# Optimization experiments

Hardware: AMD Instinct MI355X
Metric: run time of the kernel (lower is better)

Reference implementation:

```python
import jax, jax.numpy as jnp
import numpy as np

B, S, D, H, E = 4, 1024, 1024, 16, 4
HD = D // H
EPS = 1e-5


def setup_inputs() -> dict:
    key = jax.random.key(0)
    ks = jax.random.split(key, 6)
    std = 0.02
    return {
        "hidden_states": jax.random.normal(ks[0], (B, S, D), dtype=jnp.float32),
        "Wr": jax.random.normal(ks[1], (D, E), dtype=jnp.float32) * std,
        "br": jnp.zeros((E,), jnp.float32),
        "ln_g": jnp.ones((E, D), jnp.float32),
        "ln_b": jnp.zeros((E, D), jnp.float32),
        "W_attn": jax.random.normal(ks[2], (E, D, 3 * D), dtype=jnp.float32) * std,
        "b_attn": jnp.zeros((E, 3 * D), jnp.float32),
        "W_proj": jax.random.normal(ks[3], (E, D, D), dtype=jnp.float32) * std,
        "b_proj": jnp.zeros((E, D), jnp.float32),
    }


def reference(hidden_states, Wr, br, ln_g, ln_b, W_attn, b_attn, W_proj, b_proj):
    b, s, d = hidden_states.shape
    x = hidden_states.reshape(b * s, d)  # [N, D]

    # naive softmax router over experts
    score = jax.nn.softmax(x @ Wr + br, axis=-1)  # [N, E]

    # LayerNorm stats are expert-independent; affine is per-expert
    mu = jnp.mean(x, axis=-1, keepdims=True)
    var = jnp.mean(jnp.square(x - mu), axis=-1, keepdims=True)
    xn = (x - mu) * jax.lax.rsqrt(var + EPS)  # [N, D]

    ln_out = xn[:, None, :] * ln_g[None] + ln_b[None]  # [N, E, D]
    qkv_all = jnp.einsum('ned,edf->nef', ln_out, W_attn) + b_attn  # [N, E, 3D]
    # weighted_qkv: scale each expert's qkv by its routing score, sum
    qkv = jnp.einsum('ne,nef->nf', score, qkv_all)  # [N, 3D]

    q, k, v = jnp.split(qkv.reshape(b, s, 3 * d), 3, axis=-1)
    def split_heads(t):
        return t.reshape(b, s, H, HD).transpose(0, 2, 1, 3)  # [B,H,S,hd]
    q, k, v = split_heads(q), split_heads(k), split_heads(v)

    scale = 1.0 / jnp.sqrt(jnp.asarray(HD, q.dtype))
    att = jnp.einsum('bhqd,bhkd->bhqk', q, k) * scale  # [B,H,S,S]
    causal = jnp.tril(jnp.ones((s, s), dtype=bool))
    att = jnp.where(causal[None, None], att, jnp.finfo(att.dtype).min)
    probs = jax.nn.softmax(att, axis=-1)
    ctx = jnp.einsum('bhqk,bhkd->bhqd', probs, v)  # [B,H,S,hd]
    ctx = ctx.transpose(0, 2, 1, 3).reshape(b * s, d)  # [N, D]

    proj_all = jnp.einsum('nd,edf->nef', ctx, W_proj) + b_proj  # [N, E, D]
    out = jnp.einsum('ne,nef->nf', score, proj_all).reshape(b, s, d)
    return out
```

## Files before the change

kernel.cpp:

```cpp
#include <hip/hip_runtime.h>
#include <stdint.h>

#define NB 4
#define SS 1024
#define DD 1024
#define EE 4
#define HH 16
#define HDD 64
#define NN (NB*SS)
#define KK2 (EE*DD)
#define FF1 (3*DD)

typedef __attribute__((ext_vector_type(4))) float f32x4;
typedef __attribute__((ext_vector_type(8))) _Float16 half8;
typedef __attribute__((ext_vector_type(4))) _Float16 half4;

static __device__ __forceinline__ f32x4 mfma16(half8 a, half8 b, f32x4 c){
  return __builtin_amdgcn_mfma_f32_16x16x32_f16(a, b, c, 0, 0, 0);
}

#define GLOAD_LDS16(gp, lp) __builtin_amdgcn_global_load_lds( \
    (const unsigned int __attribute__((address_space(1)))*)(uintptr_t)(gp), \
    (unsigned int __attribute__((address_space(3)))*)(uintptr_t)(lp), 16, 0, 0)

#define SBAR() do { asm volatile("" ::: "memory"); \
                    __builtin_amdgcn_s_barrier(); \
                    asm volatile("" ::: "memory"); } while(0)

__global__ __launch_bounds__(256) void prep_kernel(
    const float* __restrict__ x, const float* __restrict__ Wr,
    const float* __restrict__ br, float* __restrict__ score,
    float* __restrict__ ratios, _Float16* __restrict__ xnb)
{
  int n = blockIdx.x;
  int tid = threadIdx.x;
  float4 xv = ((const float4*)(x + (size_t)n*DD))[tid];
  float xa[4] = {xv.x, xv.y, xv.z, xv.w};
  float vals[6];
  vals[0] = xa[0]+xa[1]+xa[2]+xa[3];
  vals[1] = xa[0]*xa[0]+xa[1]*xa[1]+xa[2]*xa[2]+xa[3]*xa[3];
  vals[2] = vals[3] = vals[4] = vals[5] = 0.f;
  #pragma unroll
  for (int j = 0; j < 4; ++j){
    float4 w = ((const float4*)Wr)[tid*4 + j];
    vals[2] += xa[j]*w.x; vals[3] += xa[j]*w.y;
    vals[4] += xa[j]*w.z; vals[5] += xa[j]*w.w;
  }
  #pragma unroll
  for (int off = 32; off >= 1; off >>= 1)
    #pragma unroll
    for (int i = 0; i < 6; ++i)
      vals[i] += __shfl_xor(vals[i], off, 64);
  __shared__ float red[4][6];
  int wid = tid >> 6;
  if ((tid & 63) == 0){
    #pragma unroll
    for (int i = 0; i < 6; ++i) red[wid][i] = vals[i];
  }
  __syncthreads();
  float tot[6];
  #pragma unroll
  for (int i = 0; i < 6; ++i)
    tot[i] = red[0][i] + red[1][i] + red[2][i] + red[3][i];

  float mu   = tot[0] * (1.f/DD);
  float var  = tot[1] * (1.f/DD) - mu*mu;
  float rsig = rsqrtf(var + 1e-5f);
  float lg[4];
  #pragma unroll
  for (int e = 0; e < 4; ++e) lg[e] = tot[2+e] + br[e];
  float mx = fmaxf(fmaxf(lg[0], lg[1]), fmaxf(lg[2], lg[3]));
  float ex[4], esum = 0.f;
  #pragma unroll
  for (int e = 0; e < 4; ++e){ ex[e] = __expf(lg[e] - mx); esum += ex[e]; }
  if (tid < 4){
    score[n*4 + tid] = ex[tid] / esum;
    ratios[n*4 + tid] = (tid > 0) ? (ex[tid-1] / ex[tid]) : 0.f;
  }

  half4 o;
  #pragma unroll
  for (int j = 0; j < 4; ++j) o[j] = (_Float16)((xa[j] - mu) * rsig);
  *(half4*)(xnb + (size_t)n*DD + tid*4) = o;
}

template<bool AFFINE>
__global__ __launch_bounds__(256) void transpose_f16_kernel(
    const float* __restrict__ W, _Float16* __restrict__ WT, int K, int F,
    const float* __restrict__ gvec, const float* __restrict__ bvec,
    float* __restrict__ part)
{
  __shared__ float t[64][65];
  __shared__ float red2[16][64];
  int k0 = blockIdx.x * 64, f0 = blockIdx.y * 64;
  int tid = threadIdx.x;
  int r = tid >> 4, c4 = (tid & 15) * 4;
  float pf[4] = {0.f, 0.f, 0.f, 0.f};
  #pragma unroll
  for (int i = 0; i < 4; ++i){
    int k = k0 + i*16 + r;
    float4 v = *(const float4*)(W + (size_t)k*F + f0 + c4);
    if constexpr (AFFINE){
      float bk = bvec[k];
      pf[0] += bk*v.x; pf[1] += bk*v.y; pf[2] += bk*v.z; pf[3] += bk*v.w;
      float gk = gvec[k];
      v.x *= gk; v.y *= gk; v.z *= gk; v.w *= gk;
    }
    t[i*16 + r][c4+0] = v.x; t[i*16 + r][c4+1] = v.y;
    t[i*16 + r][c4+2] = v.z; t[i*16 + r][c4+3] = v.w;
  }
  if constexpr (AFFINE){
    #pragma unroll
    for (int j = 0; j < 4; ++j) red2[r][c4+j] = pf[j];
  }
  __syncthreads();
  int f = tid >> 2, seg = tid & 3;
  half8 o0, o1;
  #pragma unroll
  for (int j = 0; j < 8; ++j){
    o0[j] = (_Float16)t[seg*16 + j][f];
    o1[j] = (_Float16)t[seg*16 + 8 + j][f];
  }
  _Float16* dst = WT + (size_t)(f0 + f)*K + k0 + seg*16;
  *(half8*)dst = o0;
  *(half8*)(dst + 8) = o1;
  if constexpr (AFFINE){
    if (tid < 64){
      float s = 0.f;
      #pragma unroll
      for (int rr = 0; rr < 16; ++rr) s += red2[rr][tid];
      part[(size_t)blockIdx.x * F + f0 + tid] = s;
    }
  }
}

__global__ __launch_bounds__(256) void bb1_kernel(
    const float* __restrict__ b_attn, const float* __restrict__ part,
    float* __restrict__ BB1)
{
  int idx = blockIdx.x*256 + threadIdx.x;
  int e = idx / FF1, f = idx - e*FF1;
  float s = b_attn[idx];
  #pragma unroll
  for (int i = 0; i < 16; ++i)
    s += part[(size_t)(e*16 + i)*FF1 + f];
  BB1[idx] = s;
}

#define G1_BM 256
#define G1_BN 192
#define G1_BK 64
#define G1_T  (KK2/G1_BK)
#define G1_ABUF (G1_BM*G1_BK)
#define G1_BBUF (G1_BN*G1_BK)
#define G1_BUFSZ (G1_ABUF+G1_BBUF)

__global__ __launch_bounds__(512, 2) void gemm1_kernel(
    const _Float16* __restrict__ XN, const _Float16* __restrict__ BT,
    const float* __restrict__ score, const float* __restrict__ ratios,
    const float* __restrict__ bias, _Float16* __restrict__ C)
{
  __shared__ _Float16 smem[2*G1_BUFSZ];
  int tid = threadIdx.x;
  int lane = tid & 63, wid = tid >> 6;
  int q = lane & 15, g = lane >> 4;
  int wr = wid >> 1, wc = wid & 1;
  int xo = (q & 7) << 3;
  int bid = blockIdx.x;
  int xcd = bid & 7, li = bid >> 3;
  int m0 = (li >> 1) * G1_BM;
  int n0 = (xcd*2 + (li & 1)) * G1_BN;

  int arow[4], brow[6];
  #pragma unroll
  for (int mf = 0; mf < 4; ++mf) arow[mf] = (wr*64 + mf*16 + q)*64;
  #pragma unroll
  for (int nf = 0; nf < 6; ++nf) brow[nf] = G1_ABUF + (wc*96 + nf*16 + q)*64;
  int soff[2] = { (g*8) ^ xo, (32 + g*8) ^ xo };

  auto stageA = [&](int t, int buf, int h){
    const int d0 = (t & 15) * G1_BK;
    _Float16* sA = smem + buf*G1_BUFSZ;
    #pragma unroll
    for (int ld = 0; ld < 2; ++ld){
      int l = h*2 + ld;
      int c = l*512 + tid;
      int row = c >> 3;
      int seg = (c & 7) ^ (row & 7);
      GLOAD_LDS16(XN + (size_t)(m0 + row)*DD + d0 + seg*8,
                  sA + (l*512 + wid*64)*8);
    }
  };
  auto stageB = [&](int t, int buf){
    const int k0 = t * G1_BK;
    _Float16* sB = smem + buf*G1_BUFSZ + G1_ABUF;
    #pragma unroll
    for (int ld = 0; ld < 3; ++ld){
      int c = ld*512 + tid;
      int row = c >> 3;
      int seg = (c & 7) ^ (row & 7);
      GLOAD_LDS16(BT + (size_t)(n0 + row)*KK2 + k0 + seg*8,
                  sB + (ld*512 + wid*64)*8);
    }
  };

  f32x4 acc[4][6] = {};
  half8 af0[2][2], af2[2][2], bf[6][2];

  stageA(0, 0, 0); stageA(0, 0, 1); stageB(0, 0);

  for (int t = 0; t < G1_T-1; ++t){
    if (t && (t & 15) == 0){
      int e = t >> 4;
      #pragma unroll
      for (int mf = 0; mf < 4; ++mf)
        #pragma unroll
        for (int r = 0; r < 4; ++r){
          int gm = m0 + wr*64 + mf*16 + g*4 + r;
          float ratio = ratios[gm*4 + e];
          #pragma unroll
          for (int nf = 0; nf < 6; ++nf)
            acc[mf][nf][r] *= ratio;
        }
    }
    int buf = t & 1, nxt = buf ^ 1;
    const _Float16* base = smem + buf*G1_BUFSZ;
    stageA(t+1, nxt, 0);
    asm volatile("s_waitcnt vmcnt(2)" ::: "memory");
    SBAR();
    #pragma unroll
    for (int m = 0; m < 2; ++m)
      #pragma unroll
      for (int k = 0; k < 2; ++k)
        af0[m][k] = *(const half8*)(base + arow[m] + soff[k]);
    #pragma unroll
    for (int n = 0; n < 3; ++n)
      #pragma unroll
      for (int k = 0; k < 2; ++k)
        bf[n][k] = *(const half8*)(base + brow[n] + soff[k]);
    stageA(t+1, nxt, 1);
    __builtin_amdgcn_s_setprio(1);
    #pragma unroll
    for (int k = 0; k < 2; ++k)
      #pragma unroll
      for (int m = 0; m < 2; ++m)
        #pragma unroll
        for (int n = 0; n < 3; ++n)
          acc[m][n] = mfma16(af0[m][k], bf[n][k], acc[m][n]);
    __builtin_amdgcn_s_setprio(0);
    #pragma unroll
    for (int n = 3; n < 6; ++n)
      #pragma unroll
      for (int k = 0; k < 2; ++k)
        bf[n][k] = *(const half8*)(base + brow[n] + soff[k]);
    stageB(t+1, nxt);
    SBAR();
    __builtin_amdgcn_s_setprio(1);
    #pragma unroll
    for (int k = 0; k < 2; ++k)
      #pragma unroll
      for (int m = 0; m < 2; ++m)
        #pragma unroll
        for (int n = 3; n < 6; ++n)
          acc[m][n] = mfma16(af0[m][k], bf[n][k], acc[m][n]);
    __builtin_amdgcn_s_setprio(0);
    #pragma unroll
    for (int m = 0; m < 2; ++m)
      #pragma unroll
      for (int k = 0; k < 2; ++k)
        af2[m][k] = *(const half8*)(base + arow[2+m] + soff[k]);
    SBAR();
    __builtin_amdgcn_s_setprio(1);
    #pragma unroll
    for (int k = 0; k < 2; ++k)
      #pragma unroll
      for (int m = 0; m < 2; ++m)
        #pragma unroll
        for (int n = 3; n < 6; ++n)
          acc[2+m][n] = mfma16(af2[m][k], bf[n][k], acc[2+m][n]);
    #pragma unroll
    for (int k = 0; k < 2; ++k)
      #pragma unroll
      for (int m = 0; m < 2; ++m)
        #pragma unroll
        for (int n = 0; n < 3; ++n)
          acc[2+m][n] = mfma16(af2[m][k], bf[n][k], acc[2+m][n]);
    __builtin_amdgcn_s_setprio(0);
  }
  {
    const _Float16* base = smem + ((G1_T-1) & 1)*G1_BUFSZ;
    asm volatile("s_waitcnt vmcnt(0)" ::: "memory");
    SBAR();
    #pragma unroll
    for (int m = 0; m < 2; ++m)
      #pragma unroll
      for (int k = 0; k < 2; ++k){
        af0[m][k] = *(const half8*)(base + arow[m] + soff[k]);
        af2[m][k] = *(const half8*)(base + arow[2+m] + soff[k]);
      }
    #pragma unroll
    for (int n = 0; n < 6; ++n)
      #pragma unroll
      for (int k = 0; k < 2; ++k)
        bf[n][k] = *(const half8*)(base + brow[n] + soff[k]);
    #pragma unroll
    for (int k = 0; k < 2; ++k)
      #pragma unroll
      for (int m = 0; m < 2; ++m)
        #pragma unroll
        for (int n = 0; n < 6; ++n){
          acc[m][n]   = mfma16(af0[m][k], bf[n][k], acc[m][n]);
          acc[2+m][n] = mfma16(af2[m][k], bf[n][k], acc[2+m][n]);
        }
  }

  float bv[6][4];
  #pragma unroll
  for (int nf = 0; nf < 6; ++nf){
    int gn = n0 + wc*96 + nf*16 + q;
    #pragma unroll
    for (int e = 0; e < 4; ++e) bv[nf][e] = bias[e*FF1 + gn];
  }
  #pragma unroll
  for (int mf = 0; mf < 4; ++mf){
    #pragma unroll
    for (int r = 0; r < 4; ++r){
      int gm = m0 + wr*64 + mf*16 + g*4 + r;
      float4 sc = *(const float4*)(score + gm*4);
      #pragma unroll
      for (int nf = 0; nf < 6; ++nf){
        int gn = n0 + wc*96 + nf*16 + q;
        float v = acc[mf][nf][r]*sc.w
                + sc.x*bv[nf][0] + sc.y*bv[nf][1] + sc.z*bv[nf][2] + sc.w*bv[nf][3];
        C[(size_t)gm*FF1 + gn] = (_Float16)v;
      }
    }
  }
}

#define G2_BK 64
#define G2_ABUF (128*G2_BK)
#define G2_BUFSZ (2*G2_ABUF)

__global__ __launch_bounds__(512) void gemm2_kernel(
    const _Float16* __restrict__ CTX, const _Float16* __restrict__ BT,
    const float* __restrict__ score, const float* __restrict__ bias,
    float* __restrict__ Cout)
{
  __shared__ _Float16 smem[2*G2_BUFSZ];
  int tid = threadIdx.x;
  int lane = tid & 63, wid = tid >> 6;
  int q = lane & 15, g = lane >> 4;
  int wr = wid >> 2, wc = wid & 3;
  int xo = (q & 7) << 3;
  int bid = blockIdx.x;
  int xcd = bid >> 5, idx = bid & 31;
  int m0 = (xcd*4 + (idx >> 3)) * 128;
  int n0 = (idx & 7) * 128;

  int arow[4], brow[2];
  #pragma unroll
  for (int mf = 0; mf < 4; ++mf) arow[mf] = (wr*64 + mf*16 + q)*64;
  #pragma unroll
  for (int nf = 0; nf < 2; ++nf) brow[nf] = G2_ABUF + (wc*32 + nf*16 + q)*64;
  int soff[2] = { (g*8) ^ xo, (32 + g*8) ^ xo };

  auto stage = [&](int t, int buf){
    const int d0 = (t & 15) * G2_BK;
    const int k0 = t * G2_BK;
    _Float16* sA = smem + buf*G2_BUFSZ;
    _Float16* sB = sA + G2_ABUF;
    #pragma unroll
    for (int ld = 0; ld < 2; ++ld){
      int c = ld*512 + tid;
      int row = c >> 3;
      int seg = (c & 7) ^ (row & 7);
      GLOAD_LDS16(CTX + (size_t)(m0 + row)*DD + d0 + seg*8,
                  sA + (ld*512 + wid*64)*8);
    }
    #pragma unroll
    for (int ld = 0; ld < 2; ++ld){
      int c = ld*512 + tid;
      int row = c >> 3;
      int seg = (c & 7) ^ (row & 7);
      GLOAD_LDS16(BT + (size_t)(n0 + row)*KK2 + k0 + seg*8,
                  sB + (ld*512 + wid*64)*8);
    }
  };

  f32x4 accp[4][2] = {}, acco[4][2] = {};

  auto merge = [&](int e){
    #pragma unroll
    for (int m = 0; m < 4; ++m)
      #pragma unroll
      for (int r = 0; r < 4; ++r){
        int gm = m0 + wr*64 + m*16 + g*4 + r;
        float s = score[(size_t)gm*4 + e];
        #pragma unroll
        for (int n = 0; n < 2; ++n){
          acco[m][n][r] += s*accp[m][n][r];
          accp[m][n][r] = 0.f;
        }
      }
  };

  half8 af[4][2], bfr[2][2];
  auto reads = [&](const _Float16* base, int k){
    #pragma unroll
    for (int m = 0; m < 4; ++m)
      af[m][k] = *(const half8*)(base + arow[m] + soff[k]);
    #pragma unroll
    for (int n = 0; n < 2; ++n)
      bfr[n][k] = *(const half8*)(base + brow[n] + soff[k]);
  };
  auto mfmas = [&](int k){
    __builtin_amdgcn_s_setprio(1);
    #pragma unroll
    for (int m = 0; m < 4; ++m)
      #pragma unroll
      for (int n = 0; n < 2; ++n)
        accp[m][n] = mfma16(af[m][k], bfr[n][k], accp[m][n]);
    __builtin_amdgcn_s_setprio(0);
  };

  stage(0, 0);
  for (int t = 0; t < KK2/G2_BK - 1; ++t){
    const _Float16* base = smem + (t & 1)*G2_BUFSZ;
    stage(t+1, (t+1)&1);
    asm volatile("s_waitcnt vmcnt(4)" ::: "memory");
    SBAR();
    reads(base, 0);
    mfmas(0);
    reads(base, 1);
    SBAR();
    mfmas(1);
    if ((t & 15) == 15) merge(t >> 4);
  }
  {
    const _Float16* base = smem + ((KK2/G2_BK - 1) & 1)*G2_BUFSZ;
    asm volatile("s_waitcnt vmcnt(0)" ::: "memory");
    SBAR();
    reads(base, 0); reads(base, 1);
    mfmas(0); mfmas(1);
    merge(3);
  }

  #pragma unroll
  for (int m = 0; m < 4; ++m){
    #pragma unroll
    for (int r = 0; r < 4; ++r){
      int gm = m0 + wr*64 + m*16 + g*4 + r;
      float4 sc = *(const float4*)(score + gm*4);
      #pragma unroll
      for (int n = 0; n < 2; ++n){
        int gn = n0 + wc*32 + n*16 + q;
        float v = acco[m][n][r]
                + sc.x*bias[gn] + sc.y*bias[DD+gn]
                + sc.z*bias[2*DD+gn] + sc.w*bias[3*DD+gn];
        Cout[(size_t)gm*DD + gn] = v;
      }
    }
  }
}

__global__ __launch_bounds__(512) void attn_kernel(
    const _Float16* __restrict__ qkv, _Float16* __restrict__ ctx)
{
  __shared__ _Float16 lsK[2][64*64];
  __shared__ _Float16 lsV[2][64*64];
  __shared__ _Float16 lsP[8][16*64];
  int bh = blockIdx.x, qt = blockIdx.y;
  int b = bh >> 4, h = bh & 15;
  int tid = threadIdx.x, lane = tid & 63, wid = tid >> 6;
  int q = lane & 15, g = lane >> 4;
  int xo = (q & 7) << 3;
  int qrow0 = qt*128 + wid*16;

  half8 qf[2];
  #pragma unroll
  for (int kk = 0; kk < 2; ++kk)
    qf[kk] = *(const half8*)(qkv + ((size_t)b*SS + qrow0 + q)*FF1 + h*HDD + kk*32 + g*8);

  auto issueK = [&](int kt, int buf){
    size_t kvrow = (size_t)b*SS + kt*64;
    int row = tid >> 3, seg = (tid & 7) ^ (row & 7);
    GLOAD_LDS16(qkv + (kvrow + row)*FF1 + DD + h*HDD + seg*8,
                lsK[buf] + (size_t)(wid*64)*8);
  };
  auto issueV = [&](int kt, half8& vr){
    size_t kvrow = (size_t)b*SS + kt*64;
    vr = *(const half8*)(qkv + (kvrow + lane)*FF1 + 2*DD + h*HDD + wid*8);
  };
  auto writeV = [&](half8 vr, int buf){
    #pragma unroll
    for (int j = 0; j < 8; ++j){
      int hd = wid*8 + j;
      lsV[buf][hd*64 + (lane ^ ((hd & 7) << 3))] = vr[j];
    }
  };

  f32x4 o[4] = {};
  float mrow = -1e30f, lsum = 0.f;
  const float SC2 = 0.18033688011112042f;
  int qglob = qrow0 + q;
  int ktmax = 2*qt + 1;

  half8 vr;
  issueK(0, 0);
  issueV(0, vr);

  for (int kt = 0; kt <= ktmax; ++kt){
    int cur = kt & 1, nxt = cur ^ 1;
    int tn = (kt < ktmax) ? kt+1 : ktmax;
    asm volatile("s_waitcnt vmcnt(1)" ::: "memory");
    SBAR();

    f32x4 st[4] = {};
    #pragma unroll
    for (int i = 0; i < 4; ++i){
      #pragma unroll
      for (int kk = 0; kk < 2; ++kk){
        half8 kf = *(const half8*)(lsK[cur] + (i*16 + q)*64 + ((kk*32 + g*8) ^ xo));
        st[i] = mfma16(kf, qf[kk], st[i]);
      }
    }
    issueK(tn, nxt);
    asm volatile("s_waitcnt vmcnt(1)" ::: "memory");
    writeV(vr, cur);

    float pvv[16]; float tm = -1e30f;
    #pragma unroll
    for (int i = 0; i < 4; ++i)
      #pragma unroll
      for (int r = 0; r < 4; ++r){
        int kglob = kt*64 + i*16 + g*4 + r;
        float sv = (kglob <= qglob) ? st[i][r]*SC2 : -1e30f;
        pvv[i*4+r] = sv; tm = fmaxf(tm, sv);
      }
    tm = fmaxf(tm, __shfl_xor(tm, 16, 64));
    tm = fmaxf(tm, __shfl_xor(tm, 32, 64));
    float mnew  = fmaxf(mrow, tm);
    float alpha = exp2f(mrow - mnew);
    mrow = mnew;
    float psum = 0.f;
    _Float16 pb[16];
    #pragma unroll
    for (int i = 0; i < 16; ++i){
      float p = exp2f(pvv[i] - mnew);
      psum += p; pb[i] = (_Float16)p;
    }
    lsum = lsum*alpha + psum;
    float af4[4];
    #pragma unroll
    for (int r = 0; r < 4; ++r) af4[r] = __shfl(alpha, g*4 + r, 64);
    #pragma unroll
    for (int n = 0; n < 4; ++n)
      #pragma unroll
      for (int r = 0; r < 4; ++r) o[n][r] *= af4[r];
    issueV(tn, vr);

    asm volatile("s_waitcnt lgkmcnt(0)" ::: "memory");
    SBAR();

    #pragma unroll
    for (int i = 0; i < 4; ++i){
      half4 w4;
      w4[0]=pb[i*4+0]; w4[1]=pb[i*4+1]; w4[2]=pb[i*4+2]; w4[3]=pb[i*4+3];
      *(half4*)(&lsP[wid][q*64 + ((i*16 + g*4) ^ xo)]) = w4;
    }
    #pragma unroll
    for (int kk = 0; kk < 2; ++kk){
      half8 pf = *(const half8*)(&lsP[wid][q*64 + ((kk*32 + g*8) ^ xo)]);
      #pragma unroll
      for (int n = 0; n < 4; ++n){
        half8 vf = *(const half8*)(&lsV[cur][(n*16 + q)*64 + ((kk*32 + g*8) ^ xo)]);
        o[n] = mfma16(pf, vf, o[n]);
      }
    }
  }
  float lt = lsum + __shfl_xor(lsum, 16, 64);
  lt = lt + __shfl_xor(lt, 32, 64);
  float rinv = 1.f / lt;
  #pragma unroll
  for (int r = 0; r < 4; ++r){
    float ri = __shfl(rinv, g*4 + r, 64);
    int qg = qt*128 + wid*16 + g*4 + r;
    _Float16* obase = ctx + ((size_t)b*SS + qg)*DD + h*HDD;
    #pragma unroll
    for (int n = 0; n < 4; ++n)
      obase[n*16 + q] = (_Float16)(o[n][r] * ri);
  }
}

extern "C" void kernel_launch(void* const* d_in, const int* in_sizes, int n_in,
                              void* d_out, int out_size, void* d_ws, size_t ws_size,
                              hipStream_t stream)
{
  const float* x      = (const float*)d_in[0];
  const float* Wr     = (const float*)d_in[1];
  const float* br     = (const float*)d_in[2];
  const float* ln_g   = (const float*)d_in[3];
  const float* ln_b   = (const float*)d_in[4];
  const float* W_attn = (const float*)d_in[5];
  const float* b_attn = (const float*)d_in[6];
  const float* W_proj = (const float*)d_in[7];
  const float* b_proj = (const float*)d_in[8];
  (void)in_sizes; (void)n_in; (void)out_size; (void)ws_size;

  char* ws = (char*)d_ws;
  size_t off = 0;
  auto alloc = [&](size_t bytes) -> void* {
    void* p = ws + off; off += (bytes + 255) & ~(size_t)255; return p;
  };
  _Float16* W1gT  = (_Float16*)alloc((size_t)FF1*KK2*2);
  _Float16* W2T   = (_Float16*)alloc((size_t)DD*KK2*2);
  float*    score = (float*)   alloc((size_t)NN*4*4);
  float*    ratio = (float*)   alloc((size_t)NN*4*4);
  _Float16* xn16  = (_Float16*)alloc((size_t)NN*DD*2);
  _Float16* qkv   = (_Float16*)alloc((size_t)NN*FF1*2);
  _Float16* ctx   = (_Float16*)alloc((size_t)NN*DD*2);
  float*    part  = (float*)   alloc((size_t)(KK2/64)*FF1*4);
  float*    BB1   = (float*)   alloc((size_t)EE*FF1*4);

  hipLaunchKernelGGL((transpose_f16_kernel<true>), dim3(KK2/64, FF1/64), dim3(256), 0, stream,
                     W_attn, W1gT, KK2, FF1, ln_g, ln_b, part);
  hipLaunchKernelGGL((transpose_f16_kernel<false>), dim3(KK2/64, DD/64), dim3(256), 0, stream,
                     W_proj, W2T, KK2, DD, nullptr, nullptr, nullptr);
  hipLaunchKernelGGL(bb1_kernel, dim3(EE*FF1/256), dim3(256), 0, stream,
                     b_attn, part, BB1);
  hipLaunchKernelGGL(prep_kernel, dim3(NN), dim3(256), 0, stream,
                     x, Wr, br, score, ratio, xn16);
  hipLaunchKernelGGL(gemm1_kernel, dim3(256), dim3(512), 0, stream,
                     xn16, W1gT, score, ratio, BB1, qkv);
  hipLaunchKernelGGL(attn_kernel, dim3(NB*HH, SS/128), dim3(512), 0, stream,
                     qkv, ctx);
  hipLaunchKernelGGL(gemm2_kernel, dim3(256), dim3(512), 0, stream,
                     ctx, W2T, score, b_proj, (float*)d_out);
}
```

Before: 199.8 us.

## Software-pipeline MFMA quadrants across iterations and skip redundant softmax rescaling

In the QKV GEMM, the B fragments are split into two halves and the last MFMA quadrant of each k-step is deferred into the next iteration, so it overlaps with the next tile's LDS reads and global loads and one barrier per iteration is dropped. The projection GEMM likewise defers its second MFMA half and the expert merge by one iteration. The attention kernel skips causal masking on fully-visible key tiles, skips the output and sum rescale when no row max increased (wave-uniform vote), and raises wave priority around its MFMA blocks. These trade more register pressure and a more intricate schedule for better overlap of memory and matrix work.

```diff
diff --git a/kernel.cpp b/kernel.cpp
--- a/kernel.cpp
+++ b/kernel.cpp
@@ -205,11 +205,72 @@
   };
 
   f32x4 acc[4][6] = {};
-  half8 af0[2][2], af2[2][2], bf[6][2];
+  half8 af0[2][2], af2[2][2], bfA[3][2], bfB[3][2];
+
+  auto C1 = [&](){
+    __builtin_amdgcn_s_setprio(1);
+    #pragma unroll
+    for (int k = 0; k < 2; ++k)
+      #pragma unroll
+      for (int m = 0; m < 2; ++m)
+        #pragma unroll
+        for (int n = 0; n < 3; ++n)
+          acc[m][n] = mfma16(af0[m][k], bfA[n][k], acc[m][n]);
+    __builtin_amdgcn_s_setprio(0);
+  };
+  auto C2 = [&](){
+    __builtin_amdgcn_s_setprio(1);
+    #pragma unroll
+    for (int k = 0; k < 2; ++k)
+      #pragma unroll
+      for (int m = 0; m < 2; ++m)
+        #pragma unroll
+        for (int n = 0; n < 3; ++n)
+          acc[2+m][n] = mfma16(af2[m][k], bfA[n][k], acc[2+m][n]);
+    __builtin_amdgcn_s_setprio(0);
+  };
+  auto C3 = [&](){
+    __builtin_amdgcn_s_setprio(1);
+    #pragma unroll
+    for (int k = 0; k < 2; ++k)
+      #pragma unroll
+      for (int m = 0; m < 2; ++m)
+        #pragma unroll
+        for (int n = 0; n < 3; ++n)
+          acc[m][3+n] = mfma16(af0[m][k], bfB[n][k], acc[m][3+n]);
+    __builtin_amdgcn_s_setprio(0);
+  };
+  auto C4 = [&](){
+    __builtin_amdgcn_s_setprio(1);
+    #pragma unroll
+    for (int k = 0; k < 2; ++k)
+      #pragma unroll
+      for (int m = 0; m < 2; ++m)
+        #pragma unroll
+        for (int n = 0; n < 3; ++n)
+          acc[2+m][3+n] = mfma16(af2[m][k], bfB[n][k], acc[2+m][3+n]);
+    __builtin_amdgcn_s_setprio(0);
+  };
 
   stageA(0, 0, 0); stageA(0, 0, 1); stageB(0, 0);
 
   for (int t = 0; t < G1_T-1; ++t){
+    int buf = t & 1, nxt = buf ^ 1;
+    const _Float16* base = smem + buf*G1_BUFSZ;
+    stageA(t+1, nxt, 0);
+    asm volatile("s_waitcnt vmcnt(2)" ::: "memory");
+    SBAR();
+    #pragma unroll
+    for (int m = 0; m < 2; ++m)
+      #pragma unroll
+      for (int k = 0; k < 2; ++k)
+        af0[m][k] = *(const half8*)(base + arow[m] + soff[k]);
+    #pragma unroll
+    for (int n = 0; n < 3; ++n)
+      #pragma unroll
+      for (int k = 0; k < 2; ++k)
+        bfA[n][k] = *(const half8*)(base + brow[n] + soff[k]);
+    if (t) C4();
     if (t && (t & 15) == 0){
       int e = t >> 4;
       #pragma unroll
@@ -223,74 +284,28 @@
             acc[mf][nf][r] *= ratio;
         }
     }
-    int buf = t & 1, nxt = buf ^ 1;
-    const _Float16* base = smem + buf*G1_BUFSZ;
-    stageA(t+1, nxt, 0);
-    asm volatile("s_waitcnt vmcnt(2)" ::: "memory");
-    SBAR();
-    #pragma unroll
-    for (int m = 0; m < 2; ++m)
-      #pragma unroll
-      for (int k = 0; k < 2; ++k)
-        af0[m][k] = *(const half8*)(base + arow[m] + soff[k]);
-    #pragma unroll
-    for (int n = 0; n < 3; ++n)
-      #pragma unroll
-      for (int k = 0; k < 2; ++k)
-        bf[n][k] = *(const half8*)(base + brow[n] + soff[k]);
+    C1();
     stageA(t+1, nxt, 1);
-    __builtin_amdgcn_s_setprio(1);
-    #pragma unroll
-    for (int k = 0; k < 2; ++k)
-      #pragma unroll
-      for (int m = 0; m < 2; ++m)
-        #pragma unroll
-        for (int n = 0; n < 3; ++n)
-          acc[m][n] = mfma16(af0[m][k], bf[n][k], acc[m][n]);
-    __builtin_amdgcn_s_setprio(0);
-    #pragma unroll
-    for (int n = 3; n < 6; ++n)
-      #pragma unroll
-      for (int k = 0; k < 2; ++k)
-        bf[n][k] = *(const half8*)(base + brow[n] + soff[k]);
-    stageB(t+1, nxt);
-    SBAR();
-    __builtin_amdgcn_s_setprio(1);
-    #pragma unroll
-    for (int k = 0; k < 2; ++k)
-      #pragma unroll
-      for (int m = 0; m < 2; ++m)
-        #pragma unroll
-        for (int n = 3; n < 6; ++n)
-          acc[m][n] = mfma16(af0[m][k], bf[n][k], acc[m][n]);
-    __builtin_amdgcn_s_setprio(0);
     #pragma unroll
     for (int m = 0; m < 2; ++m)
       #pragma unroll
       for (int k = 0; k < 2; ++k)
         af2[m][k] = *(const half8*)(base + arow[2+m] + soff[k]);
-    SBAR();
-    __builtin_amdgcn_s_setprio(1);
-    #pragma unroll
-    for (int k = 0; k < 2; ++k)
-      #pragma unroll
-      for (int m = 0; m < 2; ++m)
-        #pragma unroll
-        for (int n = 3; n < 6; ++n)
-          acc[2+m][n] = mfma16(af2[m][k], bf[n][k], acc[2+m][n]);
-    #pragma unroll
-    for (int k = 0; k < 2; ++k)
-      #pragma unroll
-      for (int m = 0; m < 2; ++m)
-        #pragma unroll
-        for (int n = 0; n < 3; ++n)
-          acc[2+m][n] = mfma16(af2[m][k], bf[n][k], acc[2+m][n]);
-    __builtin_amdgcn_s_setprio(0);
+    C2();
+    stageB(t+1, nxt);
+    #pragma unroll
+    for (int n = 0; n < 3; ++n)
+      #pragma unroll
+      for (int k = 0; k < 2; ++k)
+        bfB[n][k] = *(const half8*)(base + brow[3+n] + soff[k]);
+    SBAR();
+    C3();
   }
   {
     const _Float16* base = smem + ((G1_T-1) & 1)*G1_BUFSZ;
     asm volatile("s_waitcnt vmcnt(0)" ::: "memory");
     SBAR();
+    C4();
     #pragma unroll
     for (int m = 0; m < 2; ++m)
       #pragma unroll
@@ -299,19 +314,13 @@
         af2[m][k] = *(const half8*)(base + arow[2+m] + soff[k]);
       }
     #pragma unroll
-    for (int n = 0; n < 6; ++n)
-      #pragma unroll
-      for (int k = 0; k < 2; ++k)
-        bf[n][k] = *(const half8*)(base + brow[n] + soff[k]);
-    #pragma unroll
-    for (int k = 0; k < 2; ++k)
-      #pragma unroll
-      for (int m = 0; m < 2; ++m)
-        #pragma unroll
-        for (int n = 0; n < 6; ++n){
-          acc[m][n]   = mfma16(af0[m][k], bf[n][k], acc[m][n]);
-          acc[2+m][n] = mfma16(af2[m][k], bf[n][k], acc[2+m][n]);
-        }
+    for (int n = 0; n < 3; ++n)
+      #pragma unroll
+      for (int k = 0; k < 2; ++k){
+        bfA[n][k] = *(const half8*)(base + brow[n] + soff[k]);
+        bfB[n][k] = *(const half8*)(base + brow[3+n] + soff[k]);
+      }
+    C1(); C2(); C3(); C4();
   }
 
   float bv[6][4];
@@ -431,16 +440,17 @@
     asm volatile("s_waitcnt vmcnt(4)" ::: "memory");
     SBAR();
     reads(base, 0);
+    if (t) mfmas(1);
+    if (t && (t & 15) == 0) merge((t >> 4) - 1);
     mfmas(0);
     reads(base, 1);
     SBAR();
-    mfmas(1);
-    if ((t & 15) == 15) merge(t >> 4);
   }
   {
     const _Float16* base = smem + ((KK2/G2_BK - 1) & 1)*G2_BUFSZ;
     asm volatile("s_waitcnt vmcnt(0)" ::: "memory");
     SBAR();
+    mfmas(1);
     reads(base, 0); reads(base, 1);
     mfmas(0); mfmas(1);
     merge(3);
@@ -517,6 +527,7 @@
     SBAR();
 
     f32x4 st[4] = {};
+    __builtin_amdgcn_s_setprio(1);
     #pragma unroll
     for (int i = 0; i < 4; ++i){
       #pragma unroll
@@ -525,24 +536,34 @@
         st[i] = mfma16(kf, qf[kk], st[i]);
       }
     }
+    __builtin_amdgcn_s_setprio(0);
     issueK(tn, nxt);
     asm volatile("s_waitcnt vmcnt(1)" ::: "memory");
     writeV(vr, cur);
 
     float pvv[16]; float tm = -1e30f;
-    #pragma unroll
-    for (int i = 0; i < 4; ++i)
-      #pragma unroll
-      for (int r = 0; r < 4; ++r){
-        int kglob = kt*64 + i*16 + g*4 + r;
-        float sv = (kglob <= qglob) ? st[i][r]*SC2 : -1e30f;
-        pvv[i*4+r] = sv; tm = fmaxf(tm, sv);
-      }
+    if (kt*64 + 63 > qrow0){
+      #pragma unroll
+      for (int i = 0; i < 4; ++i)
+        #pragma unroll
+        for (int r = 0; r < 4; ++r){
+          int kglob = kt*64 + i*16 + g*4 + r;
+          float sv = (kglob <= qglob) ? st[i][r]*SC2 : -1e30f;
+          pvv[i*4+r] = sv; tm = fmaxf(tm, sv);
+        }
+    } else {
+      #pragma unroll
+      for (int i = 0; i < 4; ++i)
+        #pragma unroll
+        for (int r = 0; r < 4; ++r){
+          float sv = st[i][r]*SC2;
+          pvv[i*4+r] = sv; tm = fmaxf(tm, sv);
+        }
+    }
     tm = fmaxf(tm, __shfl_xor(tm, 16, 64));
     tm = fmaxf(tm, __shfl_xor(tm, 32, 64));
-    float mnew  = fmaxf(mrow, tm);
-    float alpha = exp2f(mrow - mnew);
-    mrow = mnew;
+    bool resc = !__all(tm <= mrow);
+    float mnew = resc ? fmaxf(mrow, tm) : mrow;
     float psum = 0.f;
     _Float16 pb[16];
     #pragma unroll
@@ -550,14 +571,20 @@
       float p = exp2f(pvv[i] - mnew);
       psum += p; pb[i] = (_Float16)p;
     }
-    lsum = lsum*alpha + psum;
-    float af4[4];
-    #pragma unroll
-    for (int r = 0; r < 4; ++r) af4[r] = __shfl(alpha, g*4 + r, 64);
-    #pragma unroll
-    for (int n = 0; n < 4; ++n)
-      #pragma unroll
-      for (int r = 0; r < 4; ++r) o[n][r] *= af4[r];
+    if (resc){
+      float alpha = exp2f(mrow - mnew);
+      mrow = mnew;
+      lsum = lsum*alpha + psum;
+      float af4[4];
+      #pragma unroll
+      for (int r = 0; r < 4; ++r) af4[r] = __shfl(alpha, g*4 + r, 64);
+      #pragma unroll
+      for (int n = 0; n < 4; ++n)
+        #pragma unroll
+        for (int r = 0; r < 4; ++r) o[n][r] *= af4[r];
+    } else {
+      lsum += psum;
+    }
     issueV(tn, vr);
 
     asm volatile("s_waitcnt lgkmcnt(0)" ::: "memory");
@@ -569,6 +596,7 @@
       w4[0]=pb[i*4+0]; w4[1]=pb[i*4+1]; w4[2]=pb[i*4+2]; w4[3]=pb[i*4+3];
       *(half4*)(&lsP[wid][q*64 + ((i*16 + g*4) ^ xo)]) = w4;
     }
+    __builtin_amdgcn_s_setprio(1);
     #pragma unroll
     for (int kk = 0; kk < 2; ++kk){
       half8 pf = *(const half8*)(&lsP[wid][q*64 + ((kk*32 + g*8) ^ xo)]);
@@ -578,6 +606,7 @@
         o[n] = mfma16(pf, vf, o[n]);
       }
     }
+    __builtin_amdgcn_s_setprio(0);
   }
   float lt = lsum + __shfl_xor(lsum, 16, 64);
   lt = lt + __shfl_xor(lt, 32, 64);
```

After: 200.7 us. Within noise of the previous version (+0.5%).
